# Performance work log

Hardware: AMD Instinct MI355X
Metric: run time of the kernel (lower is better)

## Reference

```python
import jax, jax.numpy as jnp
import numpy as np

N_HEAD, D_MODEL, D_HEAD = 16, 1024, 64
QLEN, MLEN, BATCH = 1024, 1024, 4
KLEN = QLEN + MLEN
LN_EPS = 1e-5


def _rel_shift(x):
    # x: [q, r, b, n] -> Transformer-XL relative shift
    q, r = x.shape[0], x.shape[1]
    zero_pad = jnp.zeros((q, 1) + x.shape[2:], x.dtype)
    x_padded = jnp.concatenate([zero_pad, x], axis=1)  # [q, r+1, b, n]
    x_padded = x_padded.reshape((r + 1, q) + x.shape[2:])
    return x_padded[1:].reshape(x.shape)


def _layer_norm(x, gamma, beta):
    mu = jnp.mean(x, axis=-1, keepdims=True)
    var = jnp.var(x, axis=-1, keepdims=True)
    return (x - mu) * jax.lax.rsqrt(var + LN_EPS) * gamma + beta


def setup_inputs() -> dict:
    key = jax.random.key(0)
    ks = jax.random.split(key, 10)
    d, n, dh = D_MODEL, N_HEAD, D_HEAD
    content = jax.random.normal(ks[0], (QLEN, BATCH, d), jnp.float32)
    mems = jax.random.normal(ks[1], (MLEN, BATCH, d), jnp.float32)
    rel_pos = jax.random.normal(ks[2], (KLEN, d), jnp.float32)
    r_w_bias = jax.random.normal(ks[3], (n, dh), jnp.float32) * 0.02
    r_r_bias = jax.random.normal(ks[4], (n, dh), jnp.float32) * 0.02
    s = 1.0 / np.sqrt(d)
    W_qkv = jax.random.normal(ks[5], (d, 3 * n * dh), jnp.float32) * s
    W_r = jax.random.normal(ks[6], (d, n * dh), jnp.float32) * s
    W_o = jax.random.normal(ks[7], (n * dh, d), jnp.float32) * s
    ln_gamma = jnp.ones((d,), jnp.float32)
    ln_beta = jnp.zeros((d,), jnp.float32)
    # causal mask with memory: query i attends to keys j <= i + MLEN (True = masked)
    attn_mask = jnp.arange(KLEN)[None, :] > (jnp.arange(QLEN)[:, None] + MLEN)
    return {
        "content": content, "rel_pos": rel_pos, "mems": mems,
        "r_w_bias": r_w_bias, "r_r_bias": r_r_bias,
        "W_qkv": W_qkv, "W_r": W_r, "W_o": W_o,
        "ln_gamma": ln_gamma, "ln_beta": ln_beta,
        "attn_mask": attn_mask,
    }


def reference(content, rel_pos, mems, r_w_bias, r_r_bias, W_qkv, W_r, W_o, ln_gamma, ln_beta, attn_mask):
    qlen, b = content.shape[0], content.shape[1]
    n, dh = N_HEAD, D_HEAD
    scale = 1.0 / np.sqrt(dh)

    cat = jnp.concatenate([mems, content], axis=0)            # [klen, b, d]
    klen = cat.shape[0]
    w_heads = cat @ W_qkv                                     # [klen, b, 3*n*dh]
    w_q, w_k, w_v = jnp.split(w_heads, 3, axis=-1)
    w_q = w_q[-qlen:].reshape(qlen, b, n, dh)
    w_k = w_k.reshape(klen, b, n, dh)
    w_v = w_v.reshape(klen, b, n, dh)
    r_k = (rel_pos @ W_r).reshape(-1, n, dh)                  # [rlen, n, dh]

    AC = jnp.einsum('ibnd,jbnd->ijbn', w_q + r_w_bias, w_k)
    BD = _rel_shift(jnp.einsum('ibnd,jnd->ijbn', w_q + r_r_bias, r_k))
    attn_score = (AC + BD) * scale                            # [q, k, b, n]
    attn_score = jnp.where(attn_mask[:, :, None, None], -jnp.inf, attn_score)
    attn_prob = jax.nn.softmax(attn_score, axis=1)

    attn_vec = jnp.einsum('ijbn,jbnd->ibnd', attn_prob, w_v)
    attn_vec = attn_vec.reshape(qlen, b, n * dh)
    attn_out = attn_vec @ W_o                                 # [q, b, d]
    return _layer_norm(content + attn_out, ln_gamma, ln_beta)
```

## Files before the change

### kernel.cpp

```cpp
#include <hip/hip_runtime.h>

#define QLEN 1024
#define MLEN 1024
#define KLEN 2048
#define BATCH 4
#define NHEAD 16
#define DHEAD 64
#define DMODEL 1024

typedef _Float16 half8 __attribute__((ext_vector_type(8)));
typedef _Float16 half4 __attribute__((ext_vector_type(4)));
typedef float f32x4 __attribute__((ext_vector_type(4)));

#define NEG_INF (-__builtin_inff())
#define QSCALE 0.18033688011112042f

typedef __attribute__((address_space(3))) unsigned int lds_u32;
typedef __attribute__((address_space(1))) unsigned int glb_u32;

__device__ __forceinline__ void gll16(void* lds, const void* g) {
  __builtin_amdgcn_global_load_lds((const glb_u32*)g, (lds_u32*)lds, 16, 0, 0);
}

__global__ __launch_bounds__(256) void k_prep(const float* __restrict__ Wqkv,
                                              const float* __restrict__ Wr,
                                              const float* __restrict__ Wo,
                                              const float* __restrict__ rel_pos,
                                              const float* __restrict__ mems,
                                              const float* __restrict__ content,
                                              _Float16* __restrict__ WqkvT,
                                              _Float16* __restrict__ WrT,
                                              _Float16* __restrict__ WoT,
                                              _Float16* __restrict__ RelP,
                                              _Float16* __restrict__ Acat)
{
  __shared__ float T[64][65];
  const int z = blockIdx.z;
  const int tid = threadIdx.x;
  if (z == 3) {
    int nb = gridDim.x * gridDim.y;
    int bid = blockIdx.y * gridDim.x + blockIdx.x;
    for (int e = (bid * 256 + tid) * 4; e < KLEN * DMODEL; e += nb * 256 * 4) {
      float4 v = *(const float4*)(rel_pos + e);
      half4 o = { (_Float16)v.x, (_Float16)v.y, (_Float16)v.z, (_Float16)v.w };
      *(half4*)(RelP + e) = o;
    }
    return;
  }
  if (z == 4) {
    int nb = gridDim.x * gridDim.y;
    int bid = blockIdx.y * gridDim.x + blockIdx.x;
    for (int e = (bid * 256 + tid) * 4; e < 8192 * DMODEL; e += nb * 256 * 4) {
      int m = e >> 10, kk = e & 1023;
      int crow = m >> 2, bb = m & 3;
      const float* src;
      if (crow < MLEN) src = mems + (size_t)(crow * BATCH + bb) * DMODEL + kk;
      else             src = content + (size_t)((crow - MLEN) * BATCH + bb) * DMODEL + kk;
      float4 v = *(const float4*)src;
      half4 o = { (_Float16)v.x, (_Float16)v.y, (_Float16)v.z, (_Float16)v.w };
      *(half4*)(Acat + (size_t)m * DMODEL + kk) = o;
    }
    return;
  }
  const float* in; _Float16* out; int C;
  if (z == 0)      { in = Wqkv; out = WqkvT; C = 3072; }
  else if (z == 1) { if (blockIdx.x >= 16) return; in = Wr; out = WrT; C = 1024; }
  else             { if (blockIdx.x >= 16) return; in = Wo; out = WoT; C = 1024; }
  const int R = 1024;
  int c0 = blockIdx.x * 64, r0 = blockIdx.y * 64;
#pragma unroll
  for (int u = 0; u < 16; ++u) {
    int lin = u * 256 + tid;
    int rr = lin >> 6, cc = lin & 63;
    T[rr][cc] = in[(size_t)(r0 + rr) * C + c0 + cc];
  }
  __syncthreads();
#pragma unroll
  for (int u = 0; u < 16; ++u) {
    int lin = u * 256 + tid;
    int cc = lin >> 6, rr = lin & 63;
    out[(size_t)(c0 + cc) * R + r0 + rr] = (_Float16)T[rr][cc];
  }
}

__global__ __launch_bounds__(256) void k_trans_v(const _Float16* __restrict__ Vb,
                                                 _Float16* __restrict__ VbT)
{
  __shared__ _Float16 T[64][72];
  int r0 = blockIdx.x * 64;
  int bh = blockIdx.y;
  const _Float16* in = Vb + (size_t)bh * KLEN * DHEAD;
  _Float16* out = VbT + (size_t)bh * DHEAD * KLEN;
  int tid = threadIdx.x;
#pragma unroll
  for (int u = 0; u < 16; ++u) {
    int lin = u * 256 + tid;
    int rr = lin >> 6, cc = lin & 63;
    T[rr][cc] = in[(size_t)(r0 + rr) * DHEAD + cc];
  }
  __syncthreads();
#pragma unroll
  for (int u = 0; u < 16; ++u) {
    int lin = u * 256 + tid;
    int cc = lin >> 6, rr = lin & 63;
    out[(size_t)cc * KLEN + r0 + rr] = T[rr][cc];
  }
}

template<typename Epi>
__device__ __forceinline__ void gemm_tile_128(const _Float16* __restrict__ A,
                                              const _Float16* __restrict__ B,
                                              int K, int m0, int n0,
                                              _Float16* As, _Float16* Bs, Epi epi)
{
  const int tid = threadIdx.x;
  const int lane = tid & 63;
  const int wave = tid >> 6;
  const int q = lane >> 4, l16 = lane & 15;
  const int wm = wave >> 1, wn = wave & 1;
  f32x4 acc[4][4] = {};

  for (int k0 = 0; k0 < K; k0 += 32) {
    __syncthreads();
#pragma unroll
    for (int i = 0; i < 2; ++i) {
      int c = i * 256 + tid;
      int row = c >> 2, pos = c & 3;
      int col8 = pos ^ ((row >> 1) & 3);
      gll16(&As[c * 8], A + (size_t)(m0 + row) * K + k0 + col8 * 8);
      gll16(&Bs[c * 8], B + (size_t)(n0 + row) * K + k0 + col8 * 8);
    }
    __syncthreads();
    half8 a[4], b[4];
#pragma unroll
    for (int rt = 0; rt < 4; ++rt) {
      int row = wm * 64 + rt * 16 + l16;
      a[rt] = *(const half8*)&As[(row * 4 + (q ^ ((row >> 1) & 3))) * 8];
    }
#pragma unroll
    for (int ct = 0; ct < 4; ++ct) {
      int row = wn * 64 + ct * 16 + l16;
      b[ct] = *(const half8*)&Bs[(row * 4 + (q ^ ((row >> 1) & 3))) * 8];
    }
#pragma unroll
    for (int rt = 0; rt < 4; ++rt)
#pragma unroll
      for (int ct = 0; ct < 4; ++ct)
        acc[rt][ct] = __builtin_amdgcn_mfma_f32_16x16x32_f16(a[rt], b[ct], acc[rt][ct], 0, 0, 0);
  }
#pragma unroll
  for (int rt = 0; rt < 4; ++rt)
#pragma unroll
    for (int ct = 0; ct < 4; ++ct)
#pragma unroll
      for (int reg = 0; reg < 4; ++reg) {
        int m = m0 + wm * 64 + rt * 16 + q * 4 + reg;
        int nn = n0 + wn * 64 + ct * 16 + l16;
        epi(m, nn, acc[rt][ct][reg]);
      }
}

__global__ __launch_bounds__(256, 2) void k_gemm_qkv_rk(
    const _Float16* __restrict__ A, const _Float16* __restrict__ B,
    const _Float16* __restrict__ RelP, const _Float16* __restrict__ WrT,
    _Float16* __restrict__ Qw, _Float16* __restrict__ Qr,
    _Float16* __restrict__ Kb, _Float16* __restrict__ Vb,
    _Float16* __restrict__ Rk2,
    const float* __restrict__ rwb, const float* __restrict__ rrb)
{
  __shared__ __align__(16) _Float16 As[128 * 32];
  __shared__ __align__(16) _Float16 Bs[128 * 32];
  const int bx = blockIdx.x, by = blockIdx.y;
  if (by >= 64) {
    if (bx >= 8) return;
    gemm_tile_128(RelP, WrT, DMODEL, (by - 64) * 128, bx * 128, As, Bs,
      [=](int m, int nn, float v) {
        int hh = nn >> 6, dd = nn & 63;
        Rk2[((size_t)hh * KLEN + m) * DHEAD + dd] = (_Float16)v;
      });
    return;
  }
  if (bx < 8 && by < 32) return;
  const int sec = bx >> 3;
  gemm_tile_128(A, B, DMODEL, by * 128, bx * 128, As, Bs,
    [=](int m, int nn, float v) {
      int c = nn & 1023;
      int hh = c >> 6, dd = c & 63;
      int crow = m >> 2, bb = m & 3;
      int bhh = bb * NHEAD + hh;
      if (sec == 0) {
        int i = crow - MLEN;
        size_t o = ((size_t)bhh * QLEN + i) * DHEAD + dd;
        Qw[o] = (_Float16)((v + rwb[c]) * QSCALE);
        Qr[o] = (_Float16)((v + rrb[c]) * QSCALE);
      } else if (sec == 1) {
        Kb[((size_t)bhh * KLEN + crow) * DHEAD + dd] = (_Float16)v;
      } else {
        Vb[((size_t)bhh * KLEN + crow) * DHEAD + dd] = (_Float16)v;
      }
    });
}

__global__ __launch_bounds__(256, 2) void k_gemm_out(
    const _Float16* __restrict__ A, const _Float16* __restrict__ B,
    const float* __restrict__ content, float* __restrict__ Y)
{
  __shared__ __align__(16) _Float16 As[128 * 32];
  __shared__ __align__(16) _Float16 Bs[128 * 32];
  gemm_tile_128(A, B, DMODEL, blockIdx.y * 128, blockIdx.x * 128, As, Bs,
    [=](int m, int nn, float v) {
      Y[(size_t)m * DMODEL + nn] = v + content[(size_t)m * DMODEL + nn];
    });
}

__global__ __launch_bounds__(256, 3) void k_attn(
    const _Float16* __restrict__ Qw, const _Float16* __restrict__ Qr,
    const _Float16* __restrict__ Kb, const _Float16* __restrict__ VbT,
    const _Float16* __restrict__ Rk2, _Float16* __restrict__ AV)
{
  __shared__ __align__(16) _Float16 Kl[2][64 * 64];
  __shared__ __align__(16) _Float16 Vtl[2][64 * 64];
  __shared__ __align__(16) _Float16 Pl[4][16 * 64];

  const int tid = threadIdx.x;
  const int lane = tid & 63, wave = tid >> 6;
  const int q = lane >> 4, l16 = lane & 15;
  const int i0 = (15 - blockIdx.x) * 64;
  const int bh = blockIdx.y;
  const int h = bh & 15, bb = bh >> 4;

  const _Float16* Qwb = Qw + (size_t)bh * QLEN * DHEAD;
  const _Float16* Qrb = Qr + (size_t)bh * QLEN * DHEAD;
  const _Float16* Kbb = Kb + (size_t)bh * KLEN * DHEAD;
  const _Float16* Vtb = VbT + (size_t)bh * DHEAD * KLEN;
  const _Float16* Rkb = Rk2 + (size_t)h * KLEN * DHEAD;

  const int iw = i0 + wave * 16;
  const int lim = iw + 15 + MLEN;

  half8 aqw[2], aqr[2];
#pragma unroll
  for (int s = 0; s < 2; ++s) {
    size_t o = (size_t)(iw + l16) * DHEAD + s * 32 + q * 8;
    aqw[s] = *(const half8*)(Qwb + o);
    aqr[s] = *(const half8*)(Qrb + o);
  }

  f32x4 oa[4] = {};
  float l_lane[4] = {};
  _Float16* Plw = &Pl[wave][0];

  auto stage = [&](int j0s, int bufi) {
#pragma unroll
    for (int i = 0; i < 2; ++i) {
      int c = i * 256 + tid;
      int row = c >> 3;
      int col8 = (c & 7) ^ (row & 7);
      gll16(&Kl[bufi][c * 8],  Kbb + (size_t)(j0s + row) * DHEAD + col8 * 8);
      gll16(&Vtl[bufi][c * 8], Vtb + (size_t)row * KLEN + j0s + col8 * 8);
    }
  };

  const int n_jt = (i0 >> 6) + 17;
  stage(0, 0);
  for (int jt = 0; jt < n_jt; ++jt) {
    const int j0 = jt * 64;
    const int bufi = jt & 1;
    __syncthreads();

    const bool act = (j0 <= lim);
    half8 rk[5][2];
    if (act) {
      const int rs = j0 - iw + 1008;
#pragma unroll
      for (int rt = 0; rt < 5; ++rt) {
        int r = rs + rt * 16 + l16;
        int rc = r < 0 ? 0 : (r > KLEN - 1 ? KLEN - 1 : r);
        const _Float16* base = Rkb + (size_t)rc * DHEAD + q * 8;
        rk[rt][0] = *(const half8*)(base);
        rk[rt][1] = *(const half8*)(base + 32);
      }
    }
    if (jt + 1 < n_jt) stage((jt + 1) * 64, bufi ^ 1);
    if (!act) continue;

    const _Float16* Klb = Kl[bufi];
    const _Float16* Vtlb = Vtl[bufi];

    f32x4 ac[4] = {};
#pragma unroll
    for (int ct = 0; ct < 4; ++ct) {
      int row = ct * 16 + l16;
#pragma unroll
      for (int s = 0; s < 2; ++s) {
        int pos = (s * 4 + q) ^ (row & 7);
        half8 bk = *(const half8*)&Klb[(row * 8 + pos) * 8];
        ac[ct] = __builtin_amdgcn_mfma_f32_16x16x32_f16(aqw[s], bk, ac[ct], 0, 0, 0);
      }
    }

    f32x4 bd[5] = {};
#pragma unroll
    for (int rt = 0; rt < 5; ++rt) {
      bd[rt] = __builtin_amdgcn_mfma_f32_16x16x32_f16(aqr[0], rk[rt][0], bd[rt], 0, 0, 0);
      bd[rt] = __builtin_amdgcn_mfma_f32_16x16x32_f16(aqr[1], rk[rt][1], bd[rt], 0, 0, 0);
    }

    const bool boundary = (j0 + 63 > iw + MLEN);
#pragma unroll
    for (int reg = 0; reg < 4; ++reg) {
      const int m = q * 4 + reg;
      const int src = (l16 + 15 - m) & 15;
      float sh[5];
#pragma unroll
      for (int rt = 0; rt < 5; ++rt) sh[rt] = __shfl(bd[rt][reg], src, 16);
      const bool sel = (l16 > m);
      float acc = 0.f;
      if (!boundary) {
#pragma unroll
        for (int ct = 0; ct < 4; ++ct) {
          float bdv = sel ? sh[ct + 1] : sh[ct];
          float e = __builtin_amdgcn_exp2f(ac[ct][reg] + bdv);
          acc += e;
          int c = ct * 16 + l16;
          Plw[m * 64 + (((c >> 3) ^ (m & 7)) * 8) + (c & 7)] = (_Float16)e;
        }
      } else {
#pragma unroll
        for (int ct = 0; ct < 4; ++ct) {
          float bdv = sel ? sh[ct + 1] : sh[ct];
          float sv = ac[ct][reg] + bdv;
          if (j0 + ct * 16 + l16 > iw + m + MLEN) sv = NEG_INF;
          float e = __builtin_amdgcn_exp2f(sv);
          acc += e;
          int c = ct * 16 + l16;
          Plw[m * 64 + (((c >> 3) ^ (m & 7)) * 8) + (c & 7)] = (_Float16)e;
        }
      }
      l_lane[reg] += acc;
    }

    half8 ap[2];
#pragma unroll
    for (int s = 0; s < 2; ++s)
      ap[s] = *(const half8*)&Plw[l16 * 64 + (((s * 4 + q) ^ (l16 & 7)) * 8)];
#pragma unroll
    for (int t = 0; t < 4; ++t) {
      int row = t * 16 + l16;
#pragma unroll
      for (int s = 0; s < 2; ++s) {
        int pos = (s * 4 + q) ^ (row & 7);
        half8 bv = *(const half8*)&Vtlb[(row * 8 + pos) * 8];
        oa[t] = __builtin_amdgcn_mfma_f32_16x16x32_f16(ap[s], bv, oa[t], 0, 0, 0);
      }
    }
  }

  float linv[4];
#pragma unroll
  for (int reg = 0; reg < 4; ++reg) {
    float v = l_lane[reg];
    v += __shfl_xor(v, 1, 16);
    v += __shfl_xor(v, 2, 16);
    v += __shfl_xor(v, 4, 16);
    v += __shfl_xor(v, 8, 16);
    linv[reg] = 1.0f / v;
  }
#pragma unroll
  for (int t = 0; t < 4; ++t)
#pragma unroll
    for (int reg = 0; reg < 4; ++reg) {
      int ii = iw + q * 4 + reg;
      AV[(size_t)(ii * BATCH + bb) * DMODEL + h * DHEAD + t * 16 + l16] =
          (_Float16)(oa[t][reg] * linv[reg]);
    }
}

__global__ __launch_bounds__(256) void k_ln(const float* __restrict__ Y,
                                            const float* __restrict__ gamma,
                                            const float* __restrict__ beta,
                                            float* __restrict__ out)
{
  int row = blockIdx.x, tid = threadIdx.x;
  const float4 v = ((const float4*)(Y + (size_t)row * DMODEL))[tid];
  float s = v.x + v.y + v.z + v.w;
  float ss = v.x * v.x + v.y * v.y + v.z * v.z + v.w * v.w;
#pragma unroll
  for (int off = 32; off >= 1; off >>= 1) {
    s += __shfl_xor(s, off, 64);
    ss += __shfl_xor(ss, off, 64);
  }
  __shared__ float red[8];
  int wave = tid >> 6, lane = tid & 63;
  if (lane == 0) { red[wave] = s; red[4 + wave] = ss; }
  __syncthreads();
  s = red[0] + red[1] + red[2] + red[3];
  ss = red[4] + red[5] + red[6] + red[7];
  float mu = s * (1.0f / DMODEL);
  float var = ss * (1.0f / DMODEL) - mu * mu;
  float rstd = rsqrtf(var + 1e-5f);
  const float4 g = ((const float4*)gamma)[tid];
  const float4 bt = ((const float4*)beta)[tid];
  float4 o;
  o.x = (v.x - mu) * rstd * g.x + bt.x;
  o.y = (v.y - mu) * rstd * g.y + bt.y;
  o.z = (v.z - mu) * rstd * g.z + bt.z;
  o.w = (v.w - mu) * rstd * g.w + bt.w;
  ((float4*)(out + (size_t)row * DMODEL))[tid] = o;
}

extern "C" void kernel_launch(void* const* d_in, const int* in_sizes, int n_in,
                              void* d_out, int out_size, void* d_ws, size_t ws_size,
                              hipStream_t stream)
{
  (void)in_sizes; (void)n_in; (void)out_size; (void)ws_size;
  const float* content = (const float*)d_in[0];
  const float* rel_pos = (const float*)d_in[1];
  const float* mems    = (const float*)d_in[2];
  const float* rwb     = (const float*)d_in[3];
  const float* rrb     = (const float*)d_in[4];
  const float* Wqkv    = (const float*)d_in[5];
  const float* Wr      = (const float*)d_in[6];
  const float* Wo      = (const float*)d_in[7];
  const float* gamma   = (const float*)d_in[8];
  const float* beta    = (const float*)d_in[9];

  char* ws = (char*)d_ws;
  size_t off = 0;
  auto take = [&](size_t bytes) { char* p = ws + off; off += (bytes + 255) & ~(size_t)255; return p; };

  _Float16* Acat  = (_Float16*)take(8192ull * 1024 * 2);
  _Float16* WqkvT = (_Float16*)take(3072ull * 1024 * 2);
  _Float16* RelP  = (_Float16*)take(2048ull * 1024 * 2);
  _Float16* WrT   = (_Float16*)take(1024ull * 1024 * 2);
  _Float16* WoT   = (_Float16*)take(1024ull * 1024 * 2);
  _Float16* Qw    = (_Float16*)take(64ull * 1024 * 64 * 2);
  _Float16* Qr    = (_Float16*)take(64ull * 1024 * 64 * 2);
  _Float16* Kb    = (_Float16*)take(64ull * 2048 * 64 * 2);
  _Float16* Vb    = (_Float16*)take(64ull * 2048 * 64 * 2);
  _Float16* AV    = (_Float16*)take(4096ull * 1024 * 2);
  _Float16* Rk2   = (_Float16*)take(16ull * 2048 * 64 * 2);
  _Float16* VbT   = Acat;
  float*    Y     = (float*)Kb;
  float*    out   = (float*)d_out;

  k_prep<<<dim3(48, 16, 5), dim3(256), 0, stream>>>(Wqkv, Wr, Wo, rel_pos, mems, content,
                                                    WqkvT, WrT, WoT, RelP, Acat);
  k_gemm_qkv_rk<<<dim3(24, 80), dim3(256), 0, stream>>>(Acat, WqkvT, RelP, WrT,
                                                        Qw, Qr, Kb, Vb, Rk2, rwb, rrb);
  k_trans_v<<<dim3(32, 64), dim3(256), 0, stream>>>(Vb, VbT);
  k_attn<<<dim3(16, 64), dim3(256), 0, stream>>>(Qw, Qr, Kb, VbT, Rk2, AV);
  k_gemm_out<<<dim3(8, 32), dim3(256), 0, stream>>>(AV, WoT, content, Y);
  k_ln<<<dim3(4096), dim3(256), 0, stream>>>(Y, gamma, beta, out);
}
```

Measured before the change: 450.8 us.

## Software-pipeline attention: compute next tile's scores while doing current softmax/PV

Restructures the attention loop so each tile's QK^T and BD MFMAs run one iteration ahead of the softmax and PV stage. K is staged two tiles ahead and V one tile ahead in separate double buffers, and the relative-key loads are issued ahead of their use. The grid is flattened so all 64 batch-heads of the heaviest query block launch first, and occupancy is lowered from 3 to 2 blocks per CU to leave registers for the extra live state. This trades occupancy and register pressure for more overlap of MFMA, exp and memory latency inside each wave.

```diff
diff --git a/kernel.cpp b/kernel.cpp
--- a/kernel.cpp
+++ b/kernel.cpp
@@ -213,7 +213,7 @@
     });
 }
 
-__global__ __launch_bounds__(256, 3) void k_attn(
+__global__ __launch_bounds__(256, 2) void k_attn(
     const _Float16* __restrict__ Qw, const _Float16* __restrict__ Qr,
     const _Float16* __restrict__ Kb, const _Float16* __restrict__ VbT,
     const _Float16* __restrict__ Rk2, _Float16* __restrict__ AV)
@@ -225,8 +225,9 @@
   const int tid = threadIdx.x;
   const int lane = tid & 63, wave = tid >> 6;
   const int q = lane >> 4, l16 = lane & 15;
-  const int i0 = (15 - blockIdx.x) * 64;
-  const int bh = blockIdx.y;
+  const int bh = blockIdx.x & 63;
+  const int xq = blockIdx.x >> 6;
+  const int i0 = (15 - xq) * 64;
   const int h = bh & 15, bb = bh >> 4;
 
   const _Float16* Qwb = Qw + (size_t)bh * QLEN * DHEAD;
@@ -250,44 +251,36 @@
   float l_lane[4] = {};
   _Float16* Plw = &Pl[wave][0];
 
-  auto stage = [&](int j0s, int bufi) {
+  auto stageK = [&](int j0s, int bufi) {
 #pragma unroll
     for (int i = 0; i < 2; ++i) {
       int c = i * 256 + tid;
       int row = c >> 3;
       int col8 = (c & 7) ^ (row & 7);
-      gll16(&Kl[bufi][c * 8],  Kbb + (size_t)(j0s + row) * DHEAD + col8 * 8);
+      gll16(&Kl[bufi][c * 8], Kbb + (size_t)(j0s + row) * DHEAD + col8 * 8);
+    }
+  };
+  auto stageV = [&](int j0s, int bufi) {
+#pragma unroll
+    for (int i = 0; i < 2; ++i) {
+      int c = i * 256 + tid;
+      int row = c >> 3;
+      int col8 = (c & 7) ^ (row & 7);
       gll16(&Vtl[bufi][c * 8], Vtb + (size_t)row * KLEN + j0s + col8 * 8);
     }
   };
-
-  const int n_jt = (i0 >> 6) + 17;
-  stage(0, 0);
-  for (int jt = 0; jt < n_jt; ++jt) {
-    const int j0 = jt * 64;
-    const int bufi = jt & 1;
-    __syncthreads();
-
-    const bool act = (j0 <= lim);
-    half8 rk[5][2];
-    if (act) {
-      const int rs = j0 - iw + 1008;
-#pragma unroll
-      for (int rt = 0; rt < 5; ++rt) {
-        int r = rs + rt * 16 + l16;
-        int rc = r < 0 ? 0 : (r > KLEN - 1 ? KLEN - 1 : r);
-        const _Float16* base = Rkb + (size_t)rc * DHEAD + q * 8;
-        rk[rt][0] = *(const half8*)(base);
-        rk[rt][1] = *(const half8*)(base + 32);
-      }
-    }
-    if (jt + 1 < n_jt) stage((jt + 1) * 64, bufi ^ 1);
-    if (!act) continue;
-
-    const _Float16* Klb = Kl[bufi];
-    const _Float16* Vtlb = Vtl[bufi];
-
-    f32x4 ac[4] = {};
+  auto loadRK = [&](int j0t, half8 (&rk)[5][2]) {
+    const int rs = j0t - iw + 1008;
+#pragma unroll
+    for (int rt = 0; rt < 5; ++rt) {
+      int r = rs + rt * 16 + l16;
+      int rc = r < 0 ? 0 : (r > KLEN - 1 ? KLEN - 1 : r);
+      const _Float16* base = Rkb + (size_t)rc * DHEAD + q * 8;
+      rk[rt][0] = *(const half8*)(base);
+      rk[rt][1] = *(const half8*)(base + 32);
+    }
+  };
+  auto computeAC = [&](const _Float16* Klb, f32x4 (&ac)[4]) {
 #pragma unroll
     for (int ct = 0; ct < 4; ++ct) {
       int row = ct * 16 + l16;
@@ -298,62 +291,105 @@
         ac[ct] = __builtin_amdgcn_mfma_f32_16x16x32_f16(aqw[s], bk, ac[ct], 0, 0, 0);
       }
     }
-
-    f32x4 bd[5] = {};
+  };
+  auto computeBD = [&](half8 (&rk)[5][2], f32x4 (&bd)[5]) {
 #pragma unroll
     for (int rt = 0; rt < 5; ++rt) {
       bd[rt] = __builtin_amdgcn_mfma_f32_16x16x32_f16(aqr[0], rk[rt][0], bd[rt], 0, 0, 0);
       bd[rt] = __builtin_amdgcn_mfma_f32_16x16x32_f16(aqr[1], rk[rt][1], bd[rt], 0, 0, 0);
     }
-
-    const bool boundary = (j0 + 63 > iw + MLEN);
-#pragma unroll
-    for (int reg = 0; reg < 4; ++reg) {
-      const int m = q * 4 + reg;
-      const int src = (l16 + 15 - m) & 15;
-      float sh[5];
-#pragma unroll
-      for (int rt = 0; rt < 5; ++rt) sh[rt] = __shfl(bd[rt][reg], src, 16);
-      const bool sel = (l16 > m);
-      float acc = 0.f;
-      if (!boundary) {
-#pragma unroll
-        for (int ct = 0; ct < 4; ++ct) {
-          float bdv = sel ? sh[ct + 1] : sh[ct];
-          float e = __builtin_amdgcn_exp2f(ac[ct][reg] + bdv);
-          acc += e;
-          int c = ct * 16 + l16;
-          Plw[m * 64 + (((c >> 3) ^ (m & 7)) * 8) + (c & 7)] = (_Float16)e;
+  };
+
+  const int n_jt = (i0 >> 6) + 17;
+
+  stageK(0, 0);
+  stageV(0, 0);
+  __syncthreads();
+  stageK(64, 1);
+  f32x4 ac_p[4] = {}, bd_p[5] = {};
+  {
+    half8 rk0[5][2];
+    loadRK(0, rk0);
+    computeAC(Kl[0], ac_p);
+    computeBD(rk0, bd_p);
+  }
+
+  for (int jt = 0; jt < n_jt; ++jt) {
+    const int j0 = jt * 64;
+    __syncthreads();
+    if (jt + 2 < n_jt) stageK((jt + 2) * 64, jt & 1);
+    if (jt + 1 < n_jt) stageV((jt + 1) * 64, (jt + 1) & 1);
+
+    const bool act  = (j0 <= lim);
+    const bool actn = (j0 + 64 <= lim) && (jt + 1 < n_jt);
+
+    f32x4 ac_n[4] = {};
+    if (actn) computeAC(Kl[(jt + 1) & 1], ac_n);
+
+    if (act) {
+      const bool boundary = (j0 + 63 > iw + MLEN);
+#pragma unroll
+      for (int reg = 0; reg < 4; ++reg) {
+        const int m = q * 4 + reg;
+        const int src = (l16 + 15 - m) & 15;
+        float sh[5];
+#pragma unroll
+        for (int rt = 0; rt < 5; ++rt) sh[rt] = __shfl(bd_p[rt][reg], src, 16);
+        const bool sel = (l16 > m);
+        float acc = 0.f;
+        if (!boundary) {
+#pragma unroll
+          for (int ct = 0; ct < 4; ++ct) {
+            float bdv = sel ? sh[ct + 1] : sh[ct];
+            float e = __builtin_amdgcn_exp2f(ac_p[ct][reg] + bdv);
+            acc += e;
+            int c = ct * 16 + l16;
+            Plw[m * 64 + (((c >> 3) ^ (m & 7)) * 8) + (c & 7)] = (_Float16)e;
+          }
+        } else {
+#pragma unroll
+          for (int ct = 0; ct < 4; ++ct) {
+            float bdv = sel ? sh[ct + 1] : sh[ct];
+            float sv = ac_p[ct][reg] + bdv;
+            if (j0 + ct * 16 + l16 > iw + m + MLEN) sv = NEG_INF;
+            float e = __builtin_amdgcn_exp2f(sv);
+            acc += e;
+            int c = ct * 16 + l16;
+            Plw[m * 64 + (((c >> 3) ^ (m & 7)) * 8) + (c & 7)] = (_Float16)e;
+          }
         }
-      } else {
-#pragma unroll
-        for (int ct = 0; ct < 4; ++ct) {
-          float bdv = sel ? sh[ct + 1] : sh[ct];
-          float sv = ac[ct][reg] + bdv;
-          if (j0 + ct * 16 + l16 > iw + m + MLEN) sv = NEG_INF;
-          float e = __builtin_amdgcn_exp2f(sv);
-          acc += e;
-          int c = ct * 16 + l16;
-          Plw[m * 64 + (((c >> 3) ^ (m & 7)) * 8) + (c & 7)] = (_Float16)e;
+        l_lane[reg] += acc;
+      }
+    }
+
+    half8 rk[5][2];
+    if (actn) loadRK((jt + 1) * 64, rk);
+
+    if (act) {
+      half8 ap[2];
+#pragma unroll
+      for (int s = 0; s < 2; ++s)
+        ap[s] = *(const half8*)&Plw[l16 * 64 + (((s * 4 + q) ^ (l16 & 7)) * 8)];
+      const _Float16* Vtlb = Vtl[jt & 1];
+#pragma unroll
+      for (int t = 0; t < 4; ++t) {
+        int row = t * 16 + l16;
+#pragma unroll
+        for (int s = 0; s < 2; ++s) {
+          int pos = (s * 4 + q) ^ (row & 7);
+          half8 bv = *(const half8*)&Vtlb[(row * 8 + pos) * 8];
+          oa[t] = __builtin_amdgcn_mfma_f32_16x16x32_f16(ap[s], bv, oa[t], 0, 0, 0);
         }
       }
-      l_lane[reg] += acc;
-    }
-
-    half8 ap[2];
-#pragma unroll
-    for (int s = 0; s < 2; ++s)
-      ap[s] = *(const half8*)&Plw[l16 * 64 + (((s * 4 + q) ^ (l16 & 7)) * 8)];
-#pragma unroll
-    for (int t = 0; t < 4; ++t) {
-      int row = t * 16 + l16;
-#pragma unroll
-      for (int s = 0; s < 2; ++s) {
-        int pos = (s * 4 + q) ^ (row & 7);
-        half8 bv = *(const half8*)&Vtlb[(row * 8 + pos) * 8];
-        oa[t] = __builtin_amdgcn_mfma_f32_16x16x32_f16(ap[s], bv, oa[t], 0, 0, 0);
-      }
-    }
+    }
+
+    if (actn) {
+#pragma unroll
+      for (int rt = 0; rt < 5; ++rt) bd_p[rt] = f32x4{0.f, 0.f, 0.f, 0.f};
+      computeBD(rk, bd_p);
+    }
+#pragma unroll
+    for (int ct = 0; ct < 4; ++ct) ac_p[ct] = ac_n[ct];
   }
 
   float linv[4];
@@ -449,7 +485,7 @@
   k_gemm_qkv_rk<<<dim3(24, 80), dim3(256), 0, stream>>>(Acat, WqkvT, RelP, WrT,
                                                         Qw, Qr, Kb, Vb, Rk2, rwb, rrb);
   k_trans_v<<<dim3(32, 64), dim3(256), 0, stream>>>(Vb, VbT);
-  k_attn<<<dim3(16, 64), dim3(256), 0, stream>>>(Qw, Qr, Kb, VbT, Rk2, AV);
+  k_attn<<<dim3(1024), dim3(256), 0, stream>>>(Qw, Qr, Kb, VbT, Rk2, AV);
   k_gemm_out<<<dim3(8, 32), dim3(256), 0, stream>>>(AV, WoT, content, Y);
   k_ln<<<dim3(4096), dim3(256), 0, stream>>>(Y, gamma, beta, out);
 }
```

After: 395.2 us. -12.3%, faster.
